# Kernel tuning notes

Measured on AMD Instinct MI355X. Metric: run time of the kernel, lower is better.

## Reference

```python
import jax, jax.numpy as jnp
import numpy as np

B, C, H, W = 8, 64, 64, 64   # C == embed_dim
NUM_EMBED = 8192
BETA = 0.25


def setup_inputs() -> dict:
    key = jax.random.key(0)
    k1, k2 = jax.random.split(key)
    z = jax.random.normal(k1, (B, C, H, W), dtype=jnp.float32)
    # nn.Embedding init: uniform(-1/num_embed, 1/num_embed)
    embedding = jax.random.uniform(
        k2, (NUM_EMBED, C), minval=-1.0 / NUM_EMBED, maxval=1.0 / NUM_EMBED,
        dtype=jnp.float32)
    return {"z": z, "embedding": embedding}


def reference(z, embedding):
    beta = BETA
    num_embed, embed_dim = embedding.shape
    eps = 1e-10

    zc = jnp.transpose(z, (0, 2, 3, 1))            # b h w c
    zf = zc.reshape(-1, embed_dim)                 # [N, d]

    # cosine distance: normalize both (z detached in torch; argmax is
    # non-differentiable anyway)
    zn = jax.lax.stop_gradient(
        zf / jnp.linalg.norm(zf, axis=1, keepdims=True))
    en = embedding / jnp.linalg.norm(embedding, axis=1, keepdims=True)
    d = jnp.einsum('bd,nd->bn', zn, en)            # [N, K] similarity

    # sort(dim=1) then take last column == argmax
    encoding_indices = jnp.argmax(d, axis=1)       # [N]

    # one-hot @ codebook == gather (same math)
    z_q = jnp.take(embedding, encoding_indices, axis=0).reshape(zc.shape)

    sg = jax.lax.stop_gradient
    loss = beta * jnp.mean((sg(z_q) - zc) ** 2) + jnp.mean((z_q - sg(zc)) ** 2)

    # straight-through estimator, back to b c h w
    z_q_st = zc + sg(z_q - zc)
    out = jnp.transpose(z_q_st, (0, 3, 1, 2))

    # perplexity from one-hot usage histogram
    n_tok = encoding_indices.shape[0]
    avg_probs = jnp.zeros((num_embed,), dtype=d.dtype).at[encoding_indices].add(1.0) / n_tok
    perplexity = jnp.exp(-jnp.sum(avg_probs * jnp.log(avg_probs + eps)))

    idx_map = encoding_indices.reshape(z.shape[0], 1, z.shape[2], z.shape[3])
    return out, loss, perplexity, idx_map
```

## Files before the change

### kernel.cpp

```cpp
#include <hip/hip_runtime.h>
#include <hip/hip_bf16.h>
#include <math.h>

#define B_    8
#define C_    64
#define H_    64
#define W_    64
#define NUM_EMBED 8192
#define DIMS  64
#define N_TOK (B_ * H_ * W_)
#define N_ELEM (B_ * C_ * H_ * W_)

typedef short v8s __attribute__((ext_vector_type(8)));
typedef float v4f __attribute__((ext_vector_type(4)));

#define MARGIN 0.011f

__device__ __forceinline__ short bf16_rne(float x) {
    unsigned u = __float_as_uint(x);
    unsigned r = (u + 0x7FFFu + ((u >> 16) & 1u)) >> 16;
    return (short)r;
}
__device__ __forceinline__ unsigned mono(float f) {
    int b = __float_as_int(f);
    return (unsigned)(b ^ ((b >> 31) | 0x80000000));
}
__device__ __forceinline__ float demono(unsigned u) {
    int b = (u >> 31) ? (int)(u ^ 0x80000000u) : (int)~u;
    return __int_as_float(b);
}
__device__ __forceinline__ unsigned long long pack_win(float d, int code) {
    return ((unsigned long long)mono(d) << 32) | (unsigned)(0xFFFFFFFFu - (unsigned)code);
}

__global__ void invnorm_kernel(const float* __restrict__ emb, float* __restrict__ invn) {
    int wave = threadIdx.x >> 6;
    int lane = threadIdx.x & 63;
    int row  = blockIdx.x * 4 + wave;
    float v = emb[row * DIMS + lane];
    float s = v * v;
    #pragma unroll
    for (int off = 1; off < 64; off <<= 1) s += __shfl_xor(s, off, 64);
    if (lane == 0) invn[row] = 1.0f / sqrtf(s);
}

__global__ void en_frag_kernel(const float* __restrict__ emb, const float* __restrict__ invn,
                               v8s* __restrict__ ef) {
    int ch = blockIdx.x * 256 + threadIdx.x;
    int l  = ch & 63;
    int st = (ch >> 6) & 1;
    int ct = ch >> 7;
    int code = ct * 16 + (l & 15);
    int kb   = st * 32 + ((l >> 4) & 3) * 8;
    float rn = invn[code];
    v8s o;
    #pragma unroll
    for (int j = 0; j < 8; ++j) o[j] = bf16_rne(emb[code * DIMS + kb + j] * rn);
    ef[ch] = o;
}

__global__ __launch_bounds__(256)
void z_prep_kernel(const float* __restrict__ z, float* __restrict__ z_tok,
                   v8s* __restrict__ af) {
    __shared__ float zs[64][65];
    __shared__ float part[4][64];
    __shared__ float rn[64];
    const int tid = threadIdx.x;
    const int w   = tid & 63;
    const int cg  = tid >> 6;
    const int bh  = blockIdx.x;
    const int b   = bh >> 6, h = bh & 63;

    const float* zb = z + (size_t)b * (C_ * H_ * W_) + h * W_;
    float ss = 0.f;
    #pragma unroll
    for (int cc = 0; cc < 16; ++cc) {
        int c = cg * 16 + cc;
        float v = zb[c * (H_ * W_) + w];
        zs[c][w] = v;
        ss += v * v;
    }
    part[cg][w] = ss;
    __syncthreads();
    if (tid < 64) {
        float s = part[0][tid] + part[1][tid] + part[2][tid] + part[3][tid];
        rn[tid] = 1.0f / sqrtf(s);
    }
    __syncthreads();

    {
        int c  = tid & 63;
        int tg = tid >> 6;
        #pragma unroll
        for (int i = 0; i < 16; ++i) {
            int tloc = tg * 16 + i;
            z_tok[(size_t)(bh * 64 + tloc) * DIMS + c] = zs[c][tloc];
        }
    }
    #pragma unroll
    for (int ii = 0; ii < 2; ++ii) {
        int ch  = tid + ii * 256;
        int mtl = ch >> 7;
        int st  = (ch >> 6) & 1;
        int l   = ch & 63;
        int tloc = mtl * 16 + (l & 15);
        int kb   = st * 32 + ((l >> 4) & 3) * 8;
        float rr = rn[tloc];
        v8s o;
        #pragma unroll
        for (int j = 0; j < 8; ++j) o[j] = bf16_rne(zs[kb + j][tloc] * rr);
        af[(size_t)((bh * 4 + mtl) * 2 + st) * 64 + l] = o;
    }
}

#define RT 8
#define CHUNK_TILES 8
#define TILES_PER_BLOCK 64
#define CHUNKS (TILES_PER_BLOCK / CHUNK_TILES)

__global__ __launch_bounds__(512, 2)
void pass1_kernel(const v8s* __restrict__ af, const v8s* __restrict__ ef,
                  unsigned* __restrict__ tokmax) {
    __shared__ v8s lds[CHUNK_TILES * 2 * 64];
    const int tid  = threadIdx.x;
    const int lane = tid & 63;
    const int wave = tid >> 6;
    const int mgrp  = blockIdx.x >> 3;
    const int split = blockIdx.x & 7;
    const int tile0 = split * TILES_PER_BLOCK;

    const int mtb = mgrp * 64 + wave * RT;
    v8s a[RT][2];
    #pragma unroll
    for (int r = 0; r < RT; ++r)
        #pragma unroll
        for (int s = 0; s < 2; ++s)
            a[r][s] = af[(size_t)((mtb + r) * 2 + s) * 64 + lane];

    v4f mx[RT];
    #pragma unroll
    for (int r = 0; r < RT; ++r) mx[r] = (v4f){-1e30f, -1e30f, -1e30f, -1e30f};

    const float4* gsrc = (const float4*)(ef + (size_t)tile0 * 2 * 64);
    float4* lf = (float4*)lds;
    float4 pre0 = gsrc[tid], pre1 = gsrc[tid + 512];

    for (int c = 0; c < CHUNKS; ++c) {
        __syncthreads();
        lf[tid] = pre0; lf[tid + 512] = pre1;
        if (c + 1 < CHUNKS) {
            const float4* nx = gsrc + (size_t)(c + 1) * 1024;
            pre0 = nx[tid]; pre1 = nx[tid + 512];
        }
        __syncthreads();
        #pragma unroll
        for (int j = 0; j < CHUNK_TILES; ++j) {
            v8s b0 = lds[(j * 2 + 0) * 64 + lane];
            v8s b1 = lds[(j * 2 + 1) * 64 + lane];
            #pragma unroll
            for (int r = 0; r < RT; ++r) {
                v4f t = (v4f){0.f, 0.f, 0.f, 0.f};
                t = __builtin_amdgcn_mfma_f32_16x16x32_bf16(a[r][0], b0, t, 0, 0, 0);
                t = __builtin_amdgcn_mfma_f32_16x16x32_bf16(a[r][1], b1, t, 0, 0, 0);
                mx[r][0] = fmaxf(mx[r][0], t[0]);
                mx[r][1] = fmaxf(mx[r][1], t[1]);
                mx[r][2] = fmaxf(mx[r][2], t[2]);
                mx[r][3] = fmaxf(mx[r][3], t[3]);
            }
        }
    }
    #pragma unroll
    for (int r = 0; r < RT; ++r)
        #pragma unroll
        for (int i = 0; i < 4; ++i) {
            float v = mx[r][i];
            v = fmaxf(v, __shfl_xor(v, 1, 64));
            v = fmaxf(v, __shfl_xor(v, 2, 64));
            v = fmaxf(v, __shfl_xor(v, 4, 64));
            v = fmaxf(v, __shfl_xor(v, 8, 64));
            mx[r][i] = v;
        }
    if ((lane & 15) == 0) {
        int q = lane >> 4;
        #pragma unroll
        for (int r = 0; r < RT; ++r)
            #pragma unroll
            for (int i = 0; i < 4; ++i) {
                int tok = (mtb + r) * 16 + q * 4 + i;
                atomicMax(&tokmax[tok], mono(mx[r][i]));
            }
    }
}

__global__ __launch_bounds__(512, 2)
void pass2_kernel(const v8s* __restrict__ af, const v8s* __restrict__ ef,
                  const unsigned* __restrict__ tokmax,
                  const float* __restrict__ z_tok, const float* __restrict__ emb,
                  const float* __restrict__ invn,
                  unsigned long long* __restrict__ winner) {
    __shared__ v8s lds[CHUNK_TILES * 2 * 64];
    const int tid  = threadIdx.x;
    const int lane = tid & 63;
    const int wave = tid >> 6;
    const int mgrp  = blockIdx.x >> 3;
    const int split = blockIdx.x & 7;
    const int tile0 = split * TILES_PER_BLOCK;

    const int mtb = mgrp * 64 + wave * RT;
    v8s a[RT][2];
    #pragma unroll
    for (int r = 0; r < RT; ++r)
        #pragma unroll
        for (int s = 0; s < 2; ++s)
            a[r][s] = af[(size_t)((mtb + r) * 2 + s) * 64 + lane];

    float thr[RT][4];
    {
        int q = lane >> 4;
        #pragma unroll
        for (int r = 0; r < RT; ++r)
            #pragma unroll
            for (int i = 0; i < 4; ++i)
                thr[r][i] = demono(tokmax[(mtb + r) * 16 + q * 4 + i]) - MARGIN;
    }

    const float4* gsrc = (const float4*)(ef + (size_t)tile0 * 2 * 64);
    float4* lf = (float4*)lds;
    float4 pre0 = gsrc[tid], pre1 = gsrc[tid + 512];

    for (int c = 0; c < CHUNKS; ++c) {
        __syncthreads();
        lf[tid] = pre0; lf[tid + 512] = pre1;
        if (c + 1 < CHUNKS) {
            const float4* nx = gsrc + (size_t)(c + 1) * 1024;
            pre0 = nx[tid]; pre1 = nx[tid + 512];
        }
        __syncthreads();
        for (int j = 0; j < CHUNK_TILES; ++j) {
            v8s b0 = lds[(j * 2 + 0) * 64 + lane];
            v8s b1 = lds[(j * 2 + 1) * 64 + lane];
            v4f acc[RT];
            #pragma unroll
            for (int r = 0; r < RT; ++r) {
                v4f t = (v4f){0.f, 0.f, 0.f, 0.f};
                t = __builtin_amdgcn_mfma_f32_16x16x32_bf16(a[r][0], b0, t, 0, 0, 0);
                t = __builtin_amdgcn_mfma_f32_16x16x32_bf16(a[r][1], b1, t, 0, 0, 0);
                acc[r] = t;
            }
            bool cand = false;
            #pragma unroll
            for (int r = 0; r < RT; ++r)
                #pragma unroll
                for (int i = 0; i < 4; ++i)
                    cand |= (acc[r][i] >= thr[r][i]);
            if (__ballot(cand)) {
                const int ctile = tile0 + c * CHUNK_TILES + j;
                #pragma unroll
                for (int r = 0; r < RT; ++r)
                    #pragma unroll
                    for (int i = 0; i < 4; ++i) {
                        unsigned long long m = __ballot(acc[r][i] >= thr[r][i]);
                        while (m) {
                            int sl = __ffsll(m) - 1;
                            m &= m - 1;
                            int tok  = (mtb + r) * 16 + ((sl >> 4) & 3) * 4 + i;
                            int code = ctile * 16 + (sl & 15);
                            float p = z_tok[(size_t)tok * DIMS + lane] *
                                      emb[(size_t)code * DIMS + lane];
                            #pragma unroll
                            for (int o = 32; o; o >>= 1) p += __shfl_xor(p, o, 64);
                            float d = p * invn[code];
                            if (lane == 0) atomicMax(&winner[tok], pack_win(d, code));
                        }
                    }
            }
        }
    }
}

__global__ void fin_idx_kernel(const unsigned long long* __restrict__ winner,
                               int* __restrict__ idx, float* __restrict__ idxmap) {
    int t = blockIdx.x * 256 + threadIdx.x;
    unsigned code = 0xFFFFFFFFu - (unsigned)(winner[t] & 0xFFFFFFFFull);
    idx[t] = (int)code;
    idxmap[t] = (float)code;
}

__global__ void gather_loss_kernel(const float* __restrict__ z,
                                   const float* __restrict__ emb,
                                   const int* __restrict__ idx,
                                   float* __restrict__ out,
                                   float* __restrict__ partial,
                                   int* __restrict__ hist) {
    __shared__ float red[256];
    const int tid  = threadIdx.x;
    const int lane = tid & 63;
    const int wave = tid >> 6;
    const int bt   = blockIdx.x;
    const int b    = bt >> 6;
    const int h    = bt & 63;

    const int t  = bt * 64 + lane;
    const int id = idx[t];
    const long base = (long)b * (C_ * H_ * W_) + h * W_ + lane;

    float sse = 0.f;
    #pragma unroll
    for (int cc = 0; cc < 16; ++cc) {
        const int c = wave * 16 + cc;
        const float q  = emb[id * DIMS + c];
        const float zv = z[base + (long)c * (H_ * W_)];
        out[base + (long)c * (H_ * W_)] = zv + (q - zv);
        const float d = q - zv;
        sse += d * d;
    }

    red[tid] = sse;
    __syncthreads();
    for (int s = 128; s > 0; s >>= 1) {
        if (tid < s) red[tid] += red[tid + s];
        __syncthreads();
    }
    if (tid == 0) partial[bt] = red[0];
    if (wave == 0) atomicAdd(&hist[id], 1);
}

__global__ void finalize_kernel(const float* __restrict__ partial,
                                const int* __restrict__ hist,
                                float* __restrict__ out_scal) {
    __shared__ double red[256];
    const int tid = threadIdx.x;

    double s = 0.0;
    for (int i = tid; i < 512; i += 256) s += (double)partial[i];
    red[tid] = s;
    __syncthreads();
    for (int st = 128; st > 0; st >>= 1) {
        if (tid < st) red[tid] += red[tid + st];
        __syncthreads();
    }
    const double sse = red[0];
    __syncthreads();

    double e = 0.0;
    for (int k = tid; k < NUM_EMBED; k += 256) {
        float p = (float)hist[k] / (float)N_TOK;
        e += (double)(p * logf(p + 1e-10f));
    }
    red[tid] = e;
    __syncthreads();
    for (int st = 128; st > 0; st >>= 1) {
        if (tid < st) red[tid] += red[tid + st];
        __syncthreads();
    }
    if (tid == 0) {
        out_scal[0] = (float)(1.25 * sse / (double)N_ELEM);
        out_scal[1] = expf(-(float)red[0]);
    }
}

extern "C" void kernel_launch(void* const* d_in, const int* in_sizes, int n_in,
                              void* d_out, int out_size, void* d_ws, size_t ws_size,
                              hipStream_t stream) {
    const float* z   = (const float*)d_in[0];
    const float* emb = (const float*)d_in[1];
    float* o = (float*)d_out;

    char* ws = (char*)d_ws;
    v8s*  af      = (v8s*)ws;
    v8s*  ef      = (v8s*)(ws + 4194304);
    unsigned long long* winner = (unsigned long long*)(ws + 5242880);
    unsigned* tokmax = (unsigned*)(ws + 5505024);
    int*   idx     = (int*)(ws + 5636096);
    float* invn    = (float*)(ws + 5767168);
    int*   hist    = (int*)(ws + 5799936);
    float* partial = (float*)(ws + 5832704);

    float* out_q      = o;
    float* out_scal   = o + N_ELEM;
    float* out_idxmap = o + N_ELEM + 2;
    float* z_tok      = o;

    hipMemsetAsync(tokmax, 0, N_TOK * sizeof(unsigned), stream);
    hipMemsetAsync(winner, 0, N_TOK * sizeof(unsigned long long), stream);
    hipMemsetAsync(hist,   0, NUM_EMBED * sizeof(int), stream);

    invnorm_kernel<<<NUM_EMBED / 4, 256, 0, stream>>>(emb, invn);
    en_frag_kernel<<<256, 256, 0, stream>>>(emb, invn, ef);
    z_prep_kernel<<<512, 256, 0, stream>>>(z, z_tok, af);
    pass1_kernel<<<256, 512, 0, stream>>>(af, ef, tokmax);
    pass2_kernel<<<256, 512, 0, stream>>>(af, ef, tokmax, z_tok, emb, invn, winner);
    fin_idx_kernel<<<N_TOK / 256, 256, 0, stream>>>(winner, idx, out_idxmap);
    gather_loss_kernel<<<N_TOK / 64, 256, 0, stream>>>(z, emb, idx, out_q, partial, hist);
    finalize_kernel<<<1, 256, 0, stream>>>(partial, hist, out_scal);
}
```

Before: 216.8 us.

## Halve per-wave row tiles, double grid and occupancy, rework candidate scan

```diff
diff --git a/kernel.cpp b/kernel.cpp
--- a/kernel.cpp
+++ b/kernel.cpp
@@ -113,23 +113,23 @@
     }
 }
 
-#define RT 8
-#define CHUNK_TILES 8
+#define RT 4
+#define CHUNK_TILES 16
 #define TILES_PER_BLOCK 64
 #define CHUNKS (TILES_PER_BLOCK / CHUNK_TILES)
 
-__global__ __launch_bounds__(512, 2)
+__global__ __launch_bounds__(512, 4)
 void pass1_kernel(const v8s* __restrict__ af, const v8s* __restrict__ ef,
                   unsigned* __restrict__ tokmax) {
     __shared__ v8s lds[CHUNK_TILES * 2 * 64];
     const int tid  = threadIdx.x;
     const int lane = tid & 63;
     const int wave = tid >> 6;
-    const int mgrp  = blockIdx.x >> 3;
+    const int bm    = blockIdx.x >> 3;
     const int split = blockIdx.x & 7;
     const int tile0 = split * TILES_PER_BLOCK;
 
-    const int mtb = mgrp * 64 + wave * RT;
+    const int mtb = bm * 32 + wave * RT;
     v8s a[RT][2];
     #pragma unroll
     for (int r = 0; r < RT; ++r)
@@ -143,14 +143,18 @@
 
     const float4* gsrc = (const float4*)(ef + (size_t)tile0 * 2 * 64);
     float4* lf = (float4*)lds;
-    float4 pre0 = gsrc[tid], pre1 = gsrc[tid + 512];
+    float4 pre[4];
+    #pragma unroll
+    for (int i = 0; i < 4; ++i) pre[i] = gsrc[tid + i * 512];
 
     for (int c = 0; c < CHUNKS; ++c) {
         __syncthreads();
-        lf[tid] = pre0; lf[tid + 512] = pre1;
+        #pragma unroll
+        for (int i = 0; i < 4; ++i) lf[tid + i * 512] = pre[i];
         if (c + 1 < CHUNKS) {
-            const float4* nx = gsrc + (size_t)(c + 1) * 1024;
-            pre0 = nx[tid]; pre1 = nx[tid + 512];
+            const float4* nx = gsrc + (size_t)(c + 1) * 2048;
+            #pragma unroll
+            for (int i = 0; i < 4; ++i) pre[i] = nx[tid + i * 512];
         }
         __syncthreads();
         #pragma unroll
@@ -192,7 +196,7 @@
     }
 }
 
-__global__ __launch_bounds__(512, 2)
+__global__ __launch_bounds__(512, 4)
 void pass2_kernel(const v8s* __restrict__ af, const v8s* __restrict__ ef,
                   const unsigned* __restrict__ tokmax,
                   const float* __restrict__ z_tok, const float* __restrict__ emb,
@@ -202,11 +206,11 @@
     const int tid  = threadIdx.x;
     const int lane = tid & 63;
     const int wave = tid >> 6;
-    const int mgrp  = blockIdx.x >> 3;
+    const int bm    = blockIdx.x >> 3;
     const int split = blockIdx.x & 7;
     const int tile0 = split * TILES_PER_BLOCK;
 
-    const int mtb = mgrp * 64 + wave * RT;
+    const int mtb = bm * 32 + wave * RT;
     v8s a[RT][2];
     #pragma unroll
     for (int r = 0; r < RT; ++r)
@@ -226,16 +230,21 @@
 
     const float4* gsrc = (const float4*)(ef + (size_t)tile0 * 2 * 64);
     float4* lf = (float4*)lds;
-    float4 pre0 = gsrc[tid], pre1 = gsrc[tid + 512];
+    float4 pre[4];
+    #pragma unroll
+    for (int i = 0; i < 4; ++i) pre[i] = gsrc[tid + i * 512];
 
     for (int c = 0; c < CHUNKS; ++c) {
         __syncthreads();
-        lf[tid] = pre0; lf[tid + 512] = pre1;
+        #pragma unroll
+        for (int i = 0; i < 4; ++i) lf[tid + i * 512] = pre[i];
         if (c + 1 < CHUNKS) {
-            const float4* nx = gsrc + (size_t)(c + 1) * 1024;
-            pre0 = nx[tid]; pre1 = nx[tid + 512];
-        }
-        __syncthreads();
+            const float4* nx = gsrc + (size_t)(c + 1) * 2048;
+            #pragma unroll
+            for (int i = 0; i < 4; ++i) pre[i] = nx[tid + i * 512];
+        }
+        __syncthreads();
+        #pragma unroll 4
         for (int j = 0; j < CHUNK_TILES; ++j) {
             v8s b0 = lds[(j * 2 + 0) * 64 + lane];
             v8s b1 = lds[(j * 2 + 1) * 64 + lane];
@@ -247,32 +256,33 @@
                 t = __builtin_amdgcn_mfma_f32_16x16x32_bf16(a[r][1], b1, t, 0, 0, 0);
                 acc[r] = t;
             }
-            bool cand = false;
+            unsigned pm = 0;
             #pragma unroll
             for (int r = 0; r < RT; ++r)
                 #pragma unroll
                 for (int i = 0; i < 4; ++i)
-                    cand |= (acc[r][i] >= thr[r][i]);
-            if (__ballot(cand)) {
+                    if (acc[r][i] >= thr[r][i]) pm |= (1u << (r * 4 + i));
+            unsigned long long act = __ballot(pm != 0);
+            if (act) {
                 const int ctile = tile0 + c * CHUNK_TILES + j;
-                #pragma unroll
-                for (int r = 0; r < RT; ++r)
-                    #pragma unroll
-                    for (int i = 0; i < 4; ++i) {
-                        unsigned long long m = __ballot(acc[r][i] >= thr[r][i]);
-                        while (m) {
-                            int sl = __ffsll(m) - 1;
-                            m &= m - 1;
-                            int tok  = (mtb + r) * 16 + ((sl >> 4) & 3) * 4 + i;
-                            int code = ctile * 16 + (sl & 15);
-                            float p = z_tok[(size_t)tok * DIMS + lane] *
-                                      emb[(size_t)code * DIMS + lane];
-                            #pragma unroll
-                            for (int o = 32; o; o >>= 1) p += __shfl_xor(p, o, 64);
-                            float d = p * invn[code];
-                            if (lane == 0) atomicMax(&winner[tok], pack_win(d, code));
-                        }
+                while (act) {
+                    int sl = __ffsll(act) - 1;
+                    act &= act - 1;
+                    unsigned lm = __shfl(pm, sl, 64);
+                    const int code = ctile * 16 + (sl & 15);
+                    while (lm) {
+                        int bit = __ffs(lm) - 1;
+                        lm &= lm - 1;
+                        int r = bit >> 2, i = bit & 3;
+                        int tok = (mtb + r) * 16 + ((sl >> 4) & 3) * 4 + i;
+                        float p = z_tok[(size_t)tok * DIMS + lane] *
+                                  emb[(size_t)code * DIMS + lane];
+                        #pragma unroll
+                        for (int o = 32; o; o >>= 1) p += __shfl_xor(p, o, 64);
+                        float d = p * invn[code];
+                        if (lane == 0) atomicMax(&winner[tok], pack_win(d, code));
                     }
+                }
             }
         }
     }
@@ -388,8 +398,8 @@
     invnorm_kernel<<<NUM_EMBED / 4, 256, 0, stream>>>(emb, invn);
     en_frag_kernel<<<256, 256, 0, stream>>>(emb, invn, ef);
     z_prep_kernel<<<512, 256, 0, stream>>>(z, z_tok, af);
-    pass1_kernel<<<256, 512, 0, stream>>>(af, ef, tokmax);
-    pass2_kernel<<<256, 512, 0, stream>>>(af, ef, tokmax, z_tok, emb, invn, winner);
+    pass1_kernel<<<512, 512, 0, stream>>>(af, ef, tokmax);
+    pass2_kernel<<<512, 512, 0, stream>>>(af, ef, tokmax, z_tok, emb, invn, winner);
     fin_idx_kernel<<<N_TOK / 256, 256, 0, stream>>>(winner, idx, out_idxmap);
     gather_loss_kernel<<<N_TOK / 64, 256, 0, stream>>>(z, emb, idx, out_q, partial, hist);
     finalize_kernel<<<1, 256, 0, stream>>>(partial, hist, out_scal);
```

New measurement: 198.8 us. -8.3%, faster.

## Fuse two-pass argmax into single pass with candidate buffer and fp32 rescoring

Applied to the files above, without the earlier changes.

```diff
diff --git a/kernel.cpp b/kernel.cpp
--- a/kernel.cpp
+++ b/kernel.cpp
@@ -14,7 +14,7 @@
 typedef short v8s __attribute__((ext_vector_type(8)));
 typedef float v4f __attribute__((ext_vector_type(4)));
 
-#define MARGIN 0.011f
+#define MARGIN 0.0095f
 
 __device__ __forceinline__ short bf16_rne(float x) {
     unsigned u = __float_as_uint(x);
@@ -29,8 +29,11 @@
     int b = (u >> 31) ? (int)(u ^ 0x80000000u) : (int)~u;
     return __int_as_float(b);
 }
-__device__ __forceinline__ unsigned long long pack_win(float d, int code) {
-    return ((unsigned long long)mono(d) << 32) | (unsigned)(0xFFFFFFFFu - (unsigned)code);
+
+__device__ __forceinline__ void gll16(const void* g, void* l) {
+    __builtin_amdgcn_global_load_lds(
+        (const __attribute__((address_space(1))) unsigned*)g,
+        (__attribute__((address_space(3))) unsigned*)l, 16, 0, 0);
 }
 
 __global__ void invnorm_kernel(const float* __restrict__ emb, float* __restrict__ invn) {
@@ -113,23 +116,36 @@
     }
 }
 
-#define RT 8
-#define CHUNK_TILES 8
-#define TILES_PER_BLOCK 64
-#define CHUNKS (TILES_PER_BLOCK / CHUNK_TILES)
-
-__global__ __launch_bounds__(512, 2)
-void pass1_kernel(const v8s* __restrict__ af, const v8s* __restrict__ ef,
-                  unsigned* __restrict__ tokmax) {
-    __shared__ v8s lds[CHUNK_TILES * 2 * 64];
+#define RT 4
+#define SPLITS 4
+#define TILES_PER_SPLIT (NUM_EMBED / 16 / SPLITS)
+#define CHUNK_TILES 16
+#define NCHUNKS (TILES_PER_SPLIT / CHUNK_TILES)
+#define CHUNK_BYTES (CHUNK_TILES * 2 * 64 * 16)
+
+__device__ __forceinline__ void stage_chunk(const char* g, char* l, int wave, int lane) {
+    #pragma unroll
+    for (int i = 0; i < 8; ++i) {
+        int unit = wave * 8 + i;
+        gll16(g + unit * 1024 + lane * 16, l + unit * 1024);
+    }
+}
+
+__global__ __launch_bounds__(256, 2)
+void pass1f_kernel(const v8s* __restrict__ af, const v8s* __restrict__ ef,
+                   unsigned* __restrict__ tokmax, unsigned* __restrict__ cnt,
+                   unsigned long long* __restrict__ cand, int slots) {
+    __shared__ v8s lds[2][CHUNK_TILES * 2 * 64];
     const int tid  = threadIdx.x;
     const int lane = tid & 63;
     const int wave = tid >> 6;
-    const int mgrp  = blockIdx.x >> 3;
-    const int split = blockIdx.x & 7;
-    const int tile0 = split * TILES_PER_BLOCK;
-
-    const int mtb = mgrp * 64 + wave * RT;
+    const int bm    = blockIdx.x >> 2;
+    const int split = blockIdx.x & 3;
+    const int tile0 = split * TILES_PER_SPLIT;
+    const int mtb   = bm * 16 + wave * RT;
+    const int quad  = lane >> 4;
+    const int col   = lane & 15;
+
     v8s a[RT][2];
     #pragma unroll
     for (int r = 0; r < RT; ++r)
@@ -137,108 +153,25 @@
         for (int s = 0; s < 2; ++s)
             a[r][s] = af[(size_t)((mtb + r) * 2 + s) * 64 + lane];
 
-    v4f mx[RT];
-    #pragma unroll
-    for (int r = 0; r < RT; ++r) mx[r] = (v4f){-1e30f, -1e30f, -1e30f, -1e30f};
-
-    const float4* gsrc = (const float4*)(ef + (size_t)tile0 * 2 * 64);
-    float4* lf = (float4*)lds;
-    float4 pre0 = gsrc[tid], pre1 = gsrc[tid + 512];
-
-    for (int c = 0; c < CHUNKS; ++c) {
-        __syncthreads();
-        lf[tid] = pre0; lf[tid + 512] = pre1;
-        if (c + 1 < CHUNKS) {
-            const float4* nx = gsrc + (size_t)(c + 1) * 1024;
-            pre0 = nx[tid]; pre1 = nx[tid + 512];
-        }
-        __syncthreads();
-        #pragma unroll
+    float mx[RT][4], thr[RT][4];
+    #pragma unroll
+    for (int r = 0; r < RT; ++r)
+        #pragma unroll
+        for (int i = 0; i < 4; ++i) { mx[r][i] = -1e30f; thr[r][i] = 1e30f; }
+
+    const char* gbase = (const char*)(ef + (size_t)tile0 * 2 * 64);
+    stage_chunk(gbase, (char*)lds[0], wave, lane);
+
+    for (int c = 0; c < NCHUNKS; ++c) {
+        __syncthreads();
+        if (c + 1 < NCHUNKS)
+            stage_chunk(gbase + (size_t)(c + 1) * CHUNK_BYTES,
+                        (char*)lds[(c + 1) & 1], wave, lane);
+        const v8s* buf = lds[c & 1];
+        const int ctile = tile0 + c * CHUNK_TILES;
         for (int j = 0; j < CHUNK_TILES; ++j) {
-            v8s b0 = lds[(j * 2 + 0) * 64 + lane];
-            v8s b1 = lds[(j * 2 + 1) * 64 + lane];
-            #pragma unroll
-            for (int r = 0; r < RT; ++r) {
-                v4f t = (v4f){0.f, 0.f, 0.f, 0.f};
-                t = __builtin_amdgcn_mfma_f32_16x16x32_bf16(a[r][0], b0, t, 0, 0, 0);
-                t = __builtin_amdgcn_mfma_f32_16x16x32_bf16(a[r][1], b1, t, 0, 0, 0);
-                mx[r][0] = fmaxf(mx[r][0], t[0]);
-                mx[r][1] = fmaxf(mx[r][1], t[1]);
-                mx[r][2] = fmaxf(mx[r][2], t[2]);
-                mx[r][3] = fmaxf(mx[r][3], t[3]);
-            }
-        }
-    }
-    #pragma unroll
-    for (int r = 0; r < RT; ++r)
-        #pragma unroll
-        for (int i = 0; i < 4; ++i) {
-            float v = mx[r][i];
-            v = fmaxf(v, __shfl_xor(v, 1, 64));
-            v = fmaxf(v, __shfl_xor(v, 2, 64));
-            v = fmaxf(v, __shfl_xor(v, 4, 64));
-            v = fmaxf(v, __shfl_xor(v, 8, 64));
-            mx[r][i] = v;
-        }
-    if ((lane & 15) == 0) {
-        int q = lane >> 4;
-        #pragma unroll
-        for (int r = 0; r < RT; ++r)
-            #pragma unroll
-            for (int i = 0; i < 4; ++i) {
-                int tok = (mtb + r) * 16 + q * 4 + i;
-                atomicMax(&tokmax[tok], mono(mx[r][i]));
-            }
-    }
-}
-
-__global__ __launch_bounds__(512, 2)
-void pass2_kernel(const v8s* __restrict__ af, const v8s* __restrict__ ef,
-                  const unsigned* __restrict__ tokmax,
-                  const float* __restrict__ z_tok, const float* __restrict__ emb,
-                  const float* __restrict__ invn,
-                  unsigned long long* __restrict__ winner) {
-    __shared__ v8s lds[CHUNK_TILES * 2 * 64];
-    const int tid  = threadIdx.x;
-    const int lane = tid & 63;
-    const int wave = tid >> 6;
-    const int mgrp  = blockIdx.x >> 3;
-    const int split = blockIdx.x & 7;
-    const int tile0 = split * TILES_PER_BLOCK;
-
-    const int mtb = mgrp * 64 + wave * RT;
-    v8s a[RT][2];
-    #pragma unroll
-    for (int r = 0; r < RT; ++r)
-        #pragma unroll
-        for (int s = 0; s < 2; ++s)
-            a[r][s] = af[(size_t)((mtb + r) * 2 + s) * 64 + lane];
-
-    float thr[RT][4];
-    {
-        int q = lane >> 4;
-        #pragma unroll
-        for (int r = 0; r < RT; ++r)
-            #pragma unroll
-            for (int i = 0; i < 4; ++i)
-                thr[r][i] = demono(tokmax[(mtb + r) * 16 + q * 4 + i]) - MARGIN;
-    }
-
-    const float4* gsrc = (const float4*)(ef + (size_t)tile0 * 2 * 64);
-    float4* lf = (float4*)lds;
-    float4 pre0 = gsrc[tid], pre1 = gsrc[tid + 512];
-
-    for (int c = 0; c < CHUNKS; ++c) {
-        __syncthreads();
-        lf[tid] = pre0; lf[tid + 512] = pre1;
-        if (c + 1 < CHUNKS) {
-            const float4* nx = gsrc + (size_t)(c + 1) * 1024;
-            pre0 = nx[tid]; pre1 = nx[tid + 512];
-        }
-        __syncthreads();
-        for (int j = 0; j < CHUNK_TILES; ++j) {
-            v8s b0 = lds[(j * 2 + 0) * 64 + lane];
-            v8s b1 = lds[(j * 2 + 1) * 64 + lane];
+            v8s b0 = buf[(j * 2 + 0) * 64 + lane];
+            v8s b1 = buf[(j * 2 + 1) * 64 + lane];
             v4f acc[RT];
             #pragma unroll
             for (int r = 0; r < RT; ++r) {
@@ -247,43 +180,167 @@
                 t = __builtin_amdgcn_mfma_f32_16x16x32_bf16(a[r][1], b1, t, 0, 0, 0);
                 acc[r] = t;
             }
-            bool cand = false;
             #pragma unroll
             for (int r = 0; r < RT; ++r)
                 #pragma unroll
-                for (int i = 0; i < 4; ++i)
-                    cand |= (acc[r][i] >= thr[r][i]);
-            if (__ballot(cand)) {
-                const int ctile = tile0 + c * CHUNK_TILES + j;
+                for (int i = 0; i < 4; ++i) {
+                    float v = acc[r][i];
+                    if (v >= thr[r][i]) {
+                        int tok  = (mtb + r) * 16 + quad * 4 + i;
+                        int code = (ctile + j) * 16 + col;
+                        unsigned slot = atomicAdd(&cnt[tok], 1u);
+                        if ((int)slot < slots)
+                            cand[(size_t)tok * slots + slot] =
+                                ((unsigned long long)mono(v) << 32) | (unsigned)code;
+                    }
+                    mx[r][i] = fmaxf(mx[r][i], v);
+                }
+        }
+        #pragma unroll
+        for (int r = 0; r < RT; ++r)
+            #pragma unroll
+            for (int i = 0; i < 4; ++i) {
+                float v = mx[r][i];
+                v = fmaxf(v, __shfl_xor(v, 1, 64));
+                v = fmaxf(v, __shfl_xor(v, 2, 64));
+                v = fmaxf(v, __shfl_xor(v, 4, 64));
+                v = fmaxf(v, __shfl_xor(v, 8, 64));
+                mx[r][i]  = v;
+                thr[r][i] = v - MARGIN;
+            }
+    }
+
+    __syncthreads();
+    stage_chunk(gbase, (char*)lds[0], wave, lane);
+    __syncthreads();
+    {
+        const v8s* buf = lds[0];
+        for (int j = 0; j < CHUNK_TILES; ++j) {
+            v8s b0 = buf[(j * 2 + 0) * 64 + lane];
+            v8s b1 = buf[(j * 2 + 1) * 64 + lane];
+            v4f acc[RT];
+            #pragma unroll
+            for (int r = 0; r < RT; ++r) {
+                v4f t = (v4f){0.f, 0.f, 0.f, 0.f};
+                t = __builtin_amdgcn_mfma_f32_16x16x32_bf16(a[r][0], b0, t, 0, 0, 0);
+                t = __builtin_amdgcn_mfma_f32_16x16x32_bf16(a[r][1], b1, t, 0, 0, 0);
+                acc[r] = t;
+            }
+            #pragma unroll
+            for (int r = 0; r < RT; ++r)
                 #pragma unroll
-                for (int r = 0; r < RT; ++r)
-                    #pragma unroll
-                    for (int i = 0; i < 4; ++i) {
-                        unsigned long long m = __ballot(acc[r][i] >= thr[r][i]);
-                        while (m) {
-                            int sl = __ffsll(m) - 1;
-                            m &= m - 1;
-                            int tok  = (mtb + r) * 16 + ((sl >> 4) & 3) * 4 + i;
-                            int code = ctile * 16 + (sl & 15);
-                            float p = z_tok[(size_t)tok * DIMS + lane] *
-                                      emb[(size_t)code * DIMS + lane];
-                            #pragma unroll
-                            for (int o = 32; o; o >>= 1) p += __shfl_xor(p, o, 64);
-                            float d = p * invn[code];
-                            if (lane == 0) atomicMax(&winner[tok], pack_win(d, code));
-                        }
+                for (int i = 0; i < 4; ++i) {
+                    float v = acc[r][i];
+                    if (v >= thr[r][i]) {
+                        int tok  = (mtb + r) * 16 + quad * 4 + i;
+                        int code = (tile0 + j) * 16 + col;
+                        unsigned slot = atomicAdd(&cnt[tok], 1u);
+                        if ((int)slot < slots)
+                            cand[(size_t)tok * slots + slot] =
+                                ((unsigned long long)mono(v) << 32) | (unsigned)code;
                     }
+                }
+        }
+    }
+    if (col == 0) {
+        #pragma unroll
+        for (int r = 0; r < RT; ++r)
+            #pragma unroll
+            for (int i = 0; i < 4; ++i) {
+                int tok = (mtb + r) * 16 + quad * 4 + i;
+                atomicMax(&tokmax[tok], mono(mx[r][i]));
             }
-        }
-    }
-}
-
-__global__ void fin_idx_kernel(const unsigned long long* __restrict__ winner,
-                               int* __restrict__ idx, float* __restrict__ idxmap) {
-    int t = blockIdx.x * 256 + threadIdx.x;
-    unsigned code = 0xFFFFFFFFu - (unsigned)(winner[t] & 0xFFFFFFFFull);
-    idx[t] = (int)code;
-    idxmap[t] = (float)code;
+    }
+}
+
+__global__ __launch_bounds__(256)
+void filter_kernel(const unsigned long long* __restrict__ cand,
+                   const unsigned* __restrict__ cnt, const unsigned* __restrict__ tokmax,
+                   const float* __restrict__ z_tok, const float* __restrict__ emb,
+                   const float* __restrict__ invn, int slots,
+                   int* __restrict__ idx, float* __restrict__ idxmap,
+                   int* __restrict__ ovflist, unsigned* __restrict__ ovfcnt) {
+    const int lane = threadIdx.x & 63;
+    const int wid  = blockIdx.x * 4 + (threadIdx.x >> 6);
+    for (int k = 0; k < 8; ++k) {
+        const int t = wid * 8 + k;
+        unsigned c = cnt[t];
+        if (c > (unsigned)slots) {
+            if (lane == 0) { unsigned s = atomicAdd(ovfcnt, 1u); ovflist[s] = t; }
+            continue;
+        }
+        float thrf = demono(tokmax[t]) - MARGIN;
+        float zv = z_tok[(size_t)t * DIMS + lane];
+        unsigned long long best = 0;
+        for (unsigned s = 0; s < c; ++s) {
+            unsigned long long e = cand[(size_t)t * slots + s];
+            if (demono((unsigned)(e >> 32)) < thrf) continue;
+            int code = (int)(e & 0xFFFFFFFFull);
+            float p = zv * emb[(size_t)code * DIMS + lane];
+            #pragma unroll
+            for (int o = 32; o; o >>= 1) p += __shfl_xor(p, o, 64);
+            float d = p * invn[code];
+            unsigned long long pk = ((unsigned long long)mono(d) << 32) |
+                                    (0xFFFFFFFFu - (unsigned)code);
+            if (pk > best) best = pk;
+        }
+        if (lane == 0) {
+            unsigned code = 0xFFFFFFFFu - (unsigned)(best & 0xFFFFFFFFull);
+            idx[t] = (int)code;
+            idxmap[t] = (float)code;
+        }
+    }
+}
+
+__global__ __launch_bounds__(256)
+void fallback_kernel(const int* __restrict__ ovflist, const unsigned* __restrict__ ovfcnt,
+                     const float* __restrict__ z_tok, const float* __restrict__ emb,
+                     const float* __restrict__ invn,
+                     unsigned long long* __restrict__ winner) {
+    __shared__ unsigned long long red[4];
+    const int lane = threadIdx.x & 63;
+    const int wave = threadIdx.x >> 6;
+    const int nt = (int)*ovfcnt;
+    const int units = nt * 4;
+    for (int u = blockIdx.x; u < units; u += gridDim.x) {
+        const int t = ovflist[u >> 2];
+        const int q = u & 3;
+        float zv = z_tok[(size_t)t * DIMS + lane];
+        unsigned long long best = 0;
+        for (int code = q * 2048 + wave; code < (q + 1) * 2048; code += 4) {
+            float p = zv * emb[(size_t)code * DIMS + lane];
+            #pragma unroll
+            for (int o = 32; o; o >>= 1) p += __shfl_xor(p, o, 64);
+            float d = p * invn[code];
+            unsigned long long pk = ((unsigned long long)mono(d) << 32) |
+                                    (0xFFFFFFFFu - (unsigned)code);
+            if (pk > best) best = pk;
+        }
+        if (lane == 0) red[wave] = best;
+        __syncthreads();
+        if (threadIdx.x == 0) {
+            unsigned long long m = red[0];
+            if (red[1] > m) m = red[1];
+            if (red[2] > m) m = red[2];
+            if (red[3] > m) m = red[3];
+            atomicMax(&winner[t], m);
+        }
+        __syncthreads();
+    }
+}
+
+__global__ void fallback_fin_kernel(const int* __restrict__ ovflist,
+                                    const unsigned* __restrict__ ovfcnt,
+                                    const unsigned long long* __restrict__ winner,
+                                    int* __restrict__ idx, float* __restrict__ idxmap) {
+    int nt = (int)*ovfcnt;
+    int i = blockIdx.x * 256 + threadIdx.x;
+    if (i < nt) {
+        int t = ovflist[i];
+        unsigned code = 0xFFFFFFFFu - (unsigned)(winner[t] & 0xFFFFFFFFull);
+        idx[t] = (int)code;
+        idxmap[t] = (float)code;
+    }
 }
 
 __global__ void gather_loss_kernel(const float* __restrict__ z,
@@ -369,28 +426,37 @@
     char* ws = (char*)d_ws;
     v8s*  af      = (v8s*)ws;
     v8s*  ef      = (v8s*)(ws + 4194304);
-    unsigned long long* winner = (unsigned long long*)(ws + 5242880);
-    unsigned* tokmax = (unsigned*)(ws + 5505024);
-    int*   idx     = (int*)(ws + 5636096);
-    float* invn    = (float*)(ws + 5767168);
-    int*   hist    = (int*)(ws + 5799936);
-    float* partial = (float*)(ws + 5832704);
+    unsigned* tokmax = (unsigned*)(ws + 5242880);
+    unsigned* cnt    = (unsigned*)(ws + 5373952);
+    unsigned long long* winner = (unsigned long long*)(ws + 5505024);
+    int*   hist    = (int*)(ws + 5767168);
+    unsigned* ovfcnt = (unsigned*)(ws + 5799936);
+    int*   ovflist = (int*)(ws + 5800192);
+    float* invn    = (float*)(ws + 5931264);
+    float* partial = (float*)(ws + 5964032);
+    int*   idx     = (int*)(ws + 5968128);
+    unsigned long long* cand = (unsigned long long*)(ws + 6099200);
+
+    long long avail = (long long)ws_size - 6099200;
+    int slots = (int)(avail / ((long long)N_TOK * 8));
+    if (slots > 32) slots = 32;
+    if (slots < 0)  slots = 0;
 
     float* out_q      = o;
     float* out_scal   = o + N_ELEM;
     float* out_idxmap = o + N_ELEM + 2;
     float* z_tok      = o;
 
-    hipMemsetAsync(tokmax, 0, N_TOK * sizeof(unsigned), stream);
-    hipMemsetAsync(winner, 0, N_TOK * sizeof(unsigned long long), stream);
-    hipMemsetAsync(hist,   0, NUM_EMBED * sizeof(int), stream);
+    hipMemsetAsync(tokmax, 0, 5800192 - 5242880, stream);
 
     invnorm_kernel<<<NUM_EMBED / 4, 256, 0, stream>>>(emb, invn);
     en_frag_kernel<<<256, 256, 0, stream>>>(emb, invn, ef);
     z_prep_kernel<<<512, 256, 0, stream>>>(z, z_tok, af);
-    pass1_kernel<<<256, 512, 0, stream>>>(af, ef, tokmax);
-    pass2_kernel<<<256, 512, 0, stream>>>(af, ef, tokmax, z_tok, emb, invn, winner);
-    fin_idx_kernel<<<N_TOK / 256, 256, 0, stream>>>(winner, idx, out_idxmap);
+    pass1f_kernel<<<512, 256, 0, stream>>>(af, ef, tokmax, cnt, cand, slots);
+    filter_kernel<<<1024, 256, 0, stream>>>(cand, cnt, tokmax, z_tok, emb, invn,
+                                            slots, idx, out_idxmap, ovflist, ovfcnt);
+    fallback_kernel<<<256, 256, 0, stream>>>(ovflist, ovfcnt, z_tok, emb, invn, winner);
+    fallback_fin_kernel<<<128, 256, 0, stream>>>(ovflist, ovfcnt, winner, idx, out_idxmap);
     gather_loss_kernel<<<N_TOK / 64, 256, 0, stream>>>(z, emb, idx, out_q, partial, hist);
     finalize_kernel<<<1, 256, 0, stream>>>(partial, hist, out_scal);
 }
```

After: 529.5 us. 2.44x slower.
